# Performance work log

Measured on AMD Instinct MI355X. Metric: run time of the kernel, lower is better.

## Reference

```python
import jax, jax.numpy as jnp
import numpy as np

N_NODES = 100_000
E_OFF = 1_000_000
HID = 32
GF = 8
NF = 8
N_LAYERS = 3


def _mlp(h, W1, b1, W2, b2):
    # Linear -> ReLU -> Linear (matches MLP([in, hidden, out]))
    return jax.nn.relu(h @ W1 + b1) @ W2 + b2


def _seg_mean(v, idx, n):
    s = jax.ops.segment_sum(v, idx, num_segments=n)
    c = jax.ops.segment_sum(jnp.ones((v.shape[0], 1), v.dtype), idx, num_segments=n)
    return s / jnp.maximum(c, 1.0)


def _graphnet(x, row, col, eattr2, g, p):
    # GraphNet with global block: edge MLP -> mean-aggregate to nodes -> node MLP -> global MLP
    eW1, eb1, eW2, eb2, nW1, nb1, nW2, nb2, gW1, gb1, gW2, gb2 = p
    n, e = x.shape[0], row.shape[0]
    gE = jnp.broadcast_to(g, (e, g.shape[1]))
    e_emb = _mlp(jnp.concatenate([gE, x[row], x[col], eattr2], axis=1), eW1, eb1, eW2, eb2)
    agg = _seg_mean(e_emb, row, n)
    gN = jnp.broadcast_to(g, (n, g.shape[1]))
    n_emb = _mlp(jnp.concatenate([gN, x, agg], axis=1), nW1, nb1, nW2, nb2)
    g_new = _mlp(jnp.concatenate([n_emb.mean(0, keepdims=True), e_emb.mean(0, keepdims=True), g], axis=1),
                 gW1, gb1, gW2, gb2)
    return e_emb, n_emb, g_new


def setup_inputs() -> dict:
    key = jax.random.key(0)
    ks = jax.random.split(key, 24)
    a = jax.random.randint(ks[0], (E_OFF,), 0, N_NODES)
    b = jax.random.randint(ks[1], (E_OFF,), 0, N_NODES)
    d = jnp.arange(N_NODES)
    l_ei = jnp.stack([jnp.concatenate([jnp.maximum(a, b), d]),
                      jnp.concatenate([jnp.minimum(a, b), d])])  # lower triangular + diag
    c = jax.random.randint(ks[2], (E_OFF,), 0, N_NODES)
    e = jax.random.randint(ks[3], (E_OFF,), 0, N_NODES)
    u_ei = jnp.stack([jnp.concatenate([jnp.minimum(c, e), d]),
                      jnp.concatenate([jnp.maximum(c, e), d])])  # upper triangular + diag
    E = E_OFF + N_NODES
    x = jax.random.normal(ks[4], (N_NODES, NF), dtype=jnp.float32)
    l_attr = jax.random.normal(ks[5], (E, 1), dtype=jnp.float32)
    u_attr = jax.random.normal(ks[6], (E, 1), dtype=jnp.float32)

    def w(k, shape):
        return (jax.random.normal(k, shape, dtype=jnp.float32) / np.sqrt(shape[-2])).astype(jnp.float32)

    e_in = GF + 2 * NF + 1 + 1  # 26 (edge attr padded to 2: skip col, zeros where absent)
    n_in = GF + 1 + NF          # 17
    g_in = NF + 1 + GF          # 17
    return {
        'x': x, 'l_edge_index': l_ei, 'u_edge_index': u_ei,
        'l_edge_attr': l_attr, 'u_edge_attr': u_attr,
        'eW1': w(ks[7], (2, N_LAYERS, e_in, HID)), 'eb1': 0.01 * jax.random.normal(ks[8], (2, N_LAYERS, HID)),
        'eW2': w(ks[9], (2, N_LAYERS, HID, 1)), 'eb2': 0.01 * jax.random.normal(ks[10], (2, N_LAYERS, 1)),
        'nW1': w(ks[11], (2, N_LAYERS, n_in, HID)), 'nb1': 0.01 * jax.random.normal(ks[12], (2, N_LAYERS, HID)),
        'nW2': w(ks[13], (2, N_LAYERS, HID, NF)), 'nb2': 0.01 * jax.random.normal(ks[14], (2, N_LAYERS, NF)),
        'gW1': w(ks[15], (2, N_LAYERS, g_in, HID)), 'gb1': 0.01 * jax.random.normal(ks[16], (2, N_LAYERS, HID)),
        'gW2': w(ks[17], (2, N_LAYERS, HID, GF)), 'gb2': 0.01 * jax.random.normal(ks[18], (2, N_LAYERS, GF)),
    }


def reference(x, l_edge_index, u_edge_index, l_edge_attr, u_edge_attr,
              eW1, eb1, eW2, eb2, nW1, nb1, nW2, nb2, gW1, gb1, gW2, gb2):
    params = (eW1, eb1, eW2, eb2, nW1, nb1, nW2, nb2, gW1, gb1, gW2, gb2)
    lr, lc = l_edge_index[0], l_edge_index[1]
    ur, uc = u_edge_index[0], u_edge_index[1]
    g = jnp.zeros((1, GF), x.dtype)
    l_e, u_e = l_edge_attr, u_edge_attr
    l_a = l_edge_attr  # skip-connection edge features (original matrix values)
    zl, zu = jnp.zeros_like(l_edge_attr), jnp.zeros_like(u_edge_attr)
    for i in range(N_LAYERS):
        p1 = tuple(w[0, i] for w in params)
        p2 = tuple(w[1, i] for w in params)
        l_in = jnp.concatenate([l_e, l_a if i != 0 else zl], axis=1)  # zeros col == no skip (block 0)
        l_e, l_n, g = _graphnet(x, lr, lc, l_in, g, p1)
        u_in = jnp.concatenate([u_e, zu], axis=1)  # l2 never has skip; padded zeros col
        u_e, u_n, g = _graphnet(l_n, ur, uc, u_in, g, p2)
        # NOTE: node embeddings are NOT carried across MP blocks in the original
    l_vals = jnp.where(lr == lc, jnp.exp(l_e[:, 0]), l_e[:, 0])
    u_vals = jnp.where(ur == uc, jnp.exp(u_e[:, 0]), u_e[:, 0])
    return jnp.concatenate([l_vals, u_vals])
```

## Files before the change

kernel.cpp:

```cpp
#include <hip/hip_runtime.h>


typedef unsigned int u32;
typedef unsigned long long u64;

#define NB_SHIFT 8
#define NB_SIZE 256
#define RSTRIDE 1104

__device__ __forceinline__ float wave_sum(float v) {
#pragma unroll
    for (int off = 32; off > 0; off >>= 1) v += __shfl_down(v, off, 64);
    return v;
}


__global__ __launch_bounds__(512) void hist_kernel(
    const int* __restrict__ lr, const int* __restrict__ ur,
    u32* __restrict__ hist, int E, int B) {
    __shared__ u32 h[512];
    const int t = threadIdx.x;
    if (t < B) h[t] = 0;
    __syncthreads();
    const int s = blockIdx.y;
    const int* rows = s ? ur : lr;
    for (int i = blockIdx.x * 512 + t; i < E; i += gridDim.x * 512)
        atomicAdd(&h[rows[i] >> NB_SHIFT], 1u);
    __syncthreads();
    if (t < B && h[t]) atomicAdd(&hist[s * B + t], h[t]);
}

__global__ __launch_bounds__(512) void scan_kernel(
    const u32* __restrict__ hist, u32* __restrict__ offs,
    u32* __restrict__ cur, int B) {
    __shared__ u32 sh[512];
    const int t = threadIdx.x;
    for (int s = 0; s < 2; ++s) {
        const u32 v = (t < B) ? hist[s * B + t] : 0u;
        sh[t] = v;
        __syncthreads();
#pragma unroll
        for (int off = 1; off < 512; off <<= 1) {
            const u32 add = (t >= off) ? sh[t - off] : 0u;
            __syncthreads();
            sh[t] += add;
            __syncthreads();
        }
        const u32 exc = sh[t] - v;
        if (t < B) {
            offs[s * (B + 1) + t] = exc;
            cur[s * B + t] = exc;
        }
        if (t == 511) offs[s * (B + 1) + B] = sh[511];
        __syncthreads();
    }
}

#define SCHUNK 4096
__global__ __launch_bounds__(512) void scatter_kernel(
    const int* __restrict__ lr, const int* __restrict__ lc,
    const int* __restrict__ ur, const int* __restrict__ uc,
    const float* __restrict__ la, const float* __restrict__ ua,
    u32* __restrict__ cur, uint4* __restrict__ tmp, int E, int B) {
    __shared__ u32 lcnt[512], lbase[512];
    const int t = threadIdx.x;
    const int s = blockIdx.y;
    const int* rows = s ? ur : lr;
    const int* cols = s ? uc : lc;
    const float* attr = s ? ua : la;
    uint4* my = tmp + (size_t)s * E;
    if (t < B) lcnt[t] = 0;
    __syncthreads();
    const int base_e = blockIdx.x * SCHUNK;
#pragma unroll
    for (int k = 0; k < SCHUNK / 512; ++k) {
        const int e = base_e + k * 512 + t;
        if (e < E) atomicAdd(&lcnt[rows[e] >> NB_SHIFT], 1u);
    }
    __syncthreads();
    if (t < B) {
        const u32 c = lcnt[t];
        lbase[t] = c ? atomicAdd(&cur[s * B + t], c) : 0u;
        lcnt[t] = 0;
    }
    __syncthreads();
#pragma unroll
    for (int k = 0; k < SCHUNK / 512; ++k) {
        const int e = base_e + k * 512 + t;
        if (e < E) {
            const int r = rows[e];
            const int b = r >> NB_SHIFT;
            const u32 pos = lbase[b] + atomicAdd(&lcnt[b], 1u);
            my[pos] = make_uint4((u32)r, (u32)cols[e], (u32)e,
                                 __float_as_uint(attr[e]));
        }
    }
}


__global__ __launch_bounds__(512) void sort_kernel(
    const uint4* __restrict__ tmp, u64* __restrict__ ekeys,
    float* __restrict__ eattrs, const u32* __restrict__ offs,
    u32* __restrict__ row_offs, int E, int N, int B) {
    __shared__ u32 cnt[NB_SIZE];
    __shared__ u32 scn[NB_SIZE];
    const int t = threadIdx.x;
    const int s = blockIdx.y;
    const int b = blockIdx.x;
    const uint4* in = tmp + (size_t)s * E;
    u64* okey = ekeys + (size_t)s * E;
    float* oattr = eattrs + (size_t)s * E;
    u32* rofs = row_offs + (size_t)s * (N + 1);
    const u32 beg = offs[s * (B + 1) + b], end = offs[s * (B + 1) + b + 1];
    if (t < NB_SIZE) cnt[t] = 0;
    __syncthreads();
    for (u32 i = beg + t; i < end; i += 512)
        atomicAdd(&cnt[in[i].x & (NB_SIZE - 1)], 1u);
    __syncthreads();
    if (t < NB_SIZE) scn[t] = cnt[t];
    __syncthreads();
#pragma unroll
    for (int off = 1; off < NB_SIZE; off <<= 1) {
        u32 add = 0;
        if (t < NB_SIZE && t >= off) add = scn[t - off];
        __syncthreads();
        if (t < NB_SIZE) scn[t] += add;
        __syncthreads();
    }
    const int n0 = b << NB_SHIFT;
    if (t < NB_SIZE) {
        const u32 excl = scn[t] - cnt[t];
        if (n0 + t < N) rofs[n0 + t] = beg + excl;
        cnt[t] = excl;
    }
    if (b == 0 && t == 0) rofs[N] = (u32)E;
    __syncthreads();
    for (u32 i = beg + t; i < end; i += 512) {
        const uint4 r = in[i];
        const u32 pos = beg + atomicAdd(&cnt[r.x & (NB_SIZE - 1)], 1u);
        okey[pos] = ((u64)r.z << 34) | ((u64)(r.x & 0x1FFFFu) << 17) |
                    (u64)(r.y & 0x1FFFFu);
        oattr[pos] = __uint_as_float(r.w);
    }
}


__global__ __launch_bounds__(256) void atabx_kernel(
    const float4* __restrict__ xf, const float* __restrict__ eW1,
    float4* __restrict__ AtabL, int N) {
    const int n = blockIdx.x * 256 + threadIdx.x;
    if (n >= N) return;
    const float4 x0 = xf[2 * (size_t)n], x1 = xf[2 * (size_t)n + 1];
    const float xs[8] = {x0.x, x0.y, x0.z, x0.w, x1.x, x1.y, x1.z, x1.w};
    for (int m = 0; m < 3; ++m) {
        const float* __restrict__ WA = eW1 + (size_t)m * 832 + 8 * 32;
        float a[32];
#pragma unroll
        for (int j = 0; j < 32; ++j) a[j] = 0.0f;
#pragma unroll
        for (int k = 0; k < 8; ++k) {
            const float v = xs[k];
#pragma unroll
            for (int j = 0; j < 32; ++j) a[j] = fmaf(v, WA[k * 32 + j], a[j]);
        }
        float4* An = AtabL + (size_t)m * 8 * N + 8 * (size_t)n;
#pragma unroll
        for (int q = 0; q < 8; ++q)
            An[q] = make_float4(a[4 * q], a[4 * q + 1], a[4 * q + 2],
                                a[4 * q + 3]);
    }
}


template <bool SKIP, bool FIRST, bool GAGG, bool VALS, bool STORE, bool GCOMP>
__global__ __launch_bounds__(256) void edge_kernel(
    const u64* __restrict__ ekey,
    const float* __restrict__ eattr,
    const float4* __restrict__ Atab,
    const float4* __restrict__ xf,
    const float* __restrict__ eprev,
    const float* __restrict__ W1,
    const float* __restrict__ b1,
    const float* __restrict__ W2,
    const float* __restrict__ b2,
    const float* __restrict__ gprev,
    float* __restrict__ gout,
    const float* __restrict__ pebins,
    const float* __restrict__ pnbins,
    const float* __restrict__ gW1, const float* __restrict__ gb1,
    const float* __restrict__ gW2, const float* __restrict__ gb2,
    float* __restrict__ ebins,
    float* __restrict__ e_out,
    float* __restrict__ vals_out,
    int E, int N, float inv_E, int cpx) {
    __shared__ float gsh[8];
    __shared__ float biasE[32];
    __shared__ float wpart[4];
    const int t = threadIdx.x;
    const int lid = (blockIdx.x & 7) * cpx + (blockIdx.x >> 3);
    const int i0 = lid * 256;
    if (i0 >= E) return;

    if constexpr (GCOMP) {
        if (t < 64) {
            float nb[8];
#pragma unroll
            for (int q = 0; q < 8; ++q) nb[q] = pnbins[t * 16 + q];
            const float eb = pebins[t];
            float gin[17];
#pragma unroll
            for (int q = 0; q < 8; ++q) {
                const float s = wave_sum(nb[q]);
                gin[q] = __shfl(s, 0, 64) / (float)N;
            }
            const float es = wave_sum(eb);
            gin[8] = __shfl(es, 0, 64) * inv_E;
#pragma unroll
            for (int k = 0; k < 8; ++k) gin[9 + k] = gprev[k];
            float hv = 0.0f;
            if (t < 32) {
                hv = gb1[t];
#pragma unroll
                for (int k = 0; k < 17; ++k)
                    hv = fmaf(gin[k], gW1[k * 32 + t], hv);
                hv = fmaxf(hv, 0.0f);
            }
#pragma unroll
            for (int q = 0; q < 8; ++q) {
                const float c = (t < 32) ? hv * gW2[t * 8 + q] : 0.0f;
                const float s = wave_sum(c);
                if (t == 0) {
                    const float gv = gb2[q] + s;
                    gsh[q] = gv;
                    if (blockIdx.x == 0) gout[q] = gv;
                }
            }
        }
    } else {
        if (t < 8) gsh[t] = gprev[t];
    }
    __syncthreads();
    if (t < 32) {
        float v = b1[t];
#pragma unroll
        for (int k = 0; k < 8; ++k) v = fmaf(gsh[k], W1[k * 32 + t], v);
        biasE[t] = v;
    }
    __syncthreads();

    const int i = i0 + t;
    const bool valid = i < E;
    const int idx = valid ? i : i0;

    const u64 key = ekey[idx];
    const u32 c = (u32)key & 0x1FFFFu;
    const u32 r = (u32)(key >> 17) & 0x1FFFFu;
    float attr = 0.0f;
    if constexpr (FIRST || SKIP) attr = eattr[idx];
    float epv;
    if constexpr (FIRST) epv = attr;
    else epv = eprev[idx];
    const float4* __restrict__ Ar = Atab + 8 * (size_t)r;
    float h[32];
#pragma unroll
    for (int q = 0; q < 8; ++q) {
        const float4 av = Ar[q];
        const float4 bi = reinterpret_cast<const float4*>(biasE)[q];
        h[4 * q + 0] = bi.x + av.x; h[4 * q + 1] = bi.y + av.y;
        h[4 * q + 2] = bi.z + av.z; h[4 * q + 3] = bi.w + av.w;
    }
    const float4 xc0 = xf[2 * (size_t)c], xc1 = xf[2 * (size_t)c + 1];
    const float cx[8] = {xc0.x, xc0.y, xc0.z, xc0.w,
                         xc1.x, xc1.y, xc1.z, xc1.w};
    const float* __restrict__ Wc = W1 + 16 * 32;
#pragma unroll
    for (int k = 0; k < 8; ++k) {
        const float v = cx[k];
#pragma unroll
        for (int j = 0; j < 32; ++j) h[j] = fmaf(v, Wc[k * 32 + j], h[j]);
    }
    const float* __restrict__ W24 = W1 + 24 * 32;
#pragma unroll
    for (int j = 0; j < 32; ++j) h[j] = fmaf(epv, W24[j], h[j]);
    if constexpr (SKIP) {
        const float* __restrict__ W25 = W1 + 25 * 32;
#pragma unroll
        for (int j = 0; j < 32; ++j) h[j] = fmaf(attr, W25[j], h[j]);
    }
    float out = b2[0];
#pragma unroll
    for (int j = 0; j < 32; ++j) out = fmaf(fmaxf(h[j], 0.0f), W2[j], out);

    if (valid) {
        if constexpr (STORE) e_out[i] = out;
        if constexpr (VALS) {
            const u32 eid = (u32)(key >> 34);
            vals_out[eid] = (r == c) ? expf(out) : out;
        }
    }
    if constexpr (GAGG) {
        const float s = wave_sum(valid ? out : 0.0f);
        if ((t & 63) == 0) wpart[t >> 6] = s;
        __syncthreads();
        if (t == 0)
            atomicAdd(&ebins[lid & 63],
                      wpart[0] + wpart[1] + wpart[2] + wpart[3]);
    }
}


template <bool EVEN>
__global__ __launch_bounds__(256) void nodemlp_kernel(
    const float* __restrict__ ep,
    const u32* __restrict__ row_offs,
    const float4* __restrict__ xf,
    const float* __restrict__ g,
    const float* __restrict__ nW1, const float* __restrict__ nb1,
    const float* __restrict__ nW2, const float* __restrict__ nb2,
    float* __restrict__ n_out,
    float* __restrict__ nbins,
    const float* __restrict__ W1u,
    float4* __restrict__ AtabU,
    int N, int cpn) {
    __shared__ float biasN[32];
    __shared__ float npart[4][8];
    const int t = threadIdx.x;
    if (t < 32) {
        float v = nb1[t];
#pragma unroll
        for (int k = 0; k < 8; ++k) v = fmaf(g[k], nW1[k * 32 + t], v);
        biasN[t] = v;
    }
    __syncthreads();
    const int lid = (blockIdx.x & 7) * cpn + (blockIdx.x >> 3);
    const int n = lid * 256 + t;
    const bool active = n < N;
    const int idx = active ? n : (N - 1);
    const u32 beg = row_offs[idx], end = row_offs[idx + 1];
    float ssum = 0.0f;
    for (u32 i = beg; i < end; ++i) ssum += ep[i];
    const float agg = ssum / fmaxf((float)(end - beg), 1.0f);
    const float4 x0 = xf[2 * (size_t)idx], x1 = xf[2 * (size_t)idx + 1];
    float in[9] = {x0.x, x0.y, x0.z, x0.w, x1.x, x1.y, x1.z, x1.w, agg};
    float h[32];
#pragma unroll
    for (int j = 0; j < 8; ++j) {
        const float4 bb = reinterpret_cast<const float4*>(biasN)[j];
        h[4 * j + 0] = bb.x; h[4 * j + 1] = bb.y;
        h[4 * j + 2] = bb.z; h[4 * j + 3] = bb.w;
    }
    const float* __restrict__ Wk = nW1 + 8 * 32;
#pragma unroll
    for (int k = 0; k < 9; ++k) {
        const float v = in[k];
#pragma unroll
        for (int j = 0; j < 32; ++j) h[j] = fmaf(v, Wk[k * 32 + j], h[j]);
    }
    float o[8];
#pragma unroll
    for (int q = 0; q < 8; ++q) o[q] = nb2[q];
#pragma unroll
    for (int j = 0; j < 32; ++j) {
        const float hv = fmaxf(h[j], 0.0f);
#pragma unroll
        for (int q = 0; q < 8; ++q) o[q] = fmaf(hv, nW2[j * 8 + q], o[q]);
    }
    if constexpr (EVEN) {
        if (active) {
            reinterpret_cast<float4*>(n_out)[2 * n] =
                make_float4(o[0], o[1], o[2], o[3]);
            reinterpret_cast<float4*>(n_out)[2 * n + 1] =
                make_float4(o[4], o[5], o[6], o[7]);
            const float* __restrict__ WA = W1u + 8 * 32;
            float a[32];
#pragma unroll
            for (int j = 0; j < 32; ++j) a[j] = 0.0f;
#pragma unroll
            for (int k = 0; k < 8; ++k) {
                const float v = o[k];
#pragma unroll
                for (int j = 0; j < 32; ++j)
                    a[j] = fmaf(v, WA[k * 32 + j], a[j]);
            }
            float4* An = AtabU + 8 * (size_t)n;
#pragma unroll
            for (int q = 0; q < 8; ++q)
                An[q] = make_float4(a[4 * q], a[4 * q + 1], a[4 * q + 2],
                                    a[4 * q + 3]);
        }
    }
#pragma unroll
    for (int q = 0; q < 8; ++q) {
        const float s2 = wave_sum(active ? o[q] : 0.0f);
        if ((t & 63) == 0) npart[t >> 6][q] = s2;
    }
    __syncthreads();
    if (t < 8) {
        float a = 0.0f;
#pragma unroll
        for (int w = 0; w < 4; ++w) a += npart[w][t];
        atomicAdd(&nbins[(blockIdx.x & 63) * 16 + t], a);
    }
}

extern "C" void kernel_launch(void* const* d_in, const int* in_sizes, int n_in,
                              void* d_out, int out_size, void* d_ws,
                              size_t ws_size, hipStream_t stream) {
    const float* x = (const float*)d_in[0];
    const int* l_ei = (const int*)d_in[1];
    const int* u_ei = (const int*)d_in[2];
    const float* l_attr = (const float*)d_in[3];
    const float* u_attr = (const float*)d_in[4];
    const float* eW1 = (const float*)d_in[5];
    const float* eb1 = (const float*)d_in[6];
    const float* eW2 = (const float*)d_in[7];
    const float* eb2 = (const float*)d_in[8];
    const float* nW1 = (const float*)d_in[9];
    const float* nb1 = (const float*)d_in[10];
    const float* nW2 = (const float*)d_in[11];
    const float* nb2 = (const float*)d_in[12];
    const float* gW1 = (const float*)d_in[13];
    const float* gb1 = (const float*)d_in[14];
    const float* gW2 = (const float*)d_in[15];
    const float* gb2 = (const float*)d_in[16];

    const int E = in_sizes[3];
    const int N = in_sizes[0] / 8;
    const int B = (N + NB_SIZE - 1) >> NB_SHIFT;
    const int Ep = (E + 3) & ~3;

    u64* ekeys = (u64*)d_ws;
    float* eattrs = (float*)(ekeys + (size_t)2 * E);
    uint4* tmp = (uint4*)(eattrs + (size_t)2 * E);
    float* AtabU = (float*)tmp;
    float* l_e = AtabU + (size_t)32 * N;
    float* u_e = l_e + Ep;
    float* l_n = u_e + Ep;
    float* AtabL = (float*)(tmp + (size_t)2 * E);
    float* gslot = AtabL + (size_t)96 * N;
    u32* hist = (u32*)(gslot + 56);
    float* dyn_all = (float*)(hist + 2 * B);
    u32* offs = (u32*)(dyn_all + 5 * RSTRIDE);
    u32* cur = offs + 2 * (B + 1);
    u32* row_offs = cur + 2 * B;

    const int* lr = l_ei;
    const int* lc = l_ei + E;
    const int* ur = u_ei;
    const int* uc = u_ei + E;
    const int sg = (E + SCHUNK - 1) / SCHUNK;
    const int ng = (N + 255) / 256;
    const int ngp = (ng + 7) & ~7;
    const int cpn = ngp >> 3;
    const int eg = (E + 255) / 256;
    const int nwg8 = (eg + 7) & ~7;
    const int cpx = nwg8 >> 3;
    const float invE = 1.0f / (float)E;
    float* outL = (float*)d_out;
    float* outU = outL + E;

    hipMemsetAsync(gslot, 0, (size_t)(56 + 2 * B + 5 * RSTRIDE) * sizeof(float),
                   stream);
    hist_kernel<<<dim3(64, 2), 512, 0, stream>>>(lr, ur, hist, E, B);
    scan_kernel<<<1, 512, 0, stream>>>(hist, offs, cur, B);
    scatter_kernel<<<dim3(sg, 2), 512, 0, stream>>>(lr, lc, ur, uc, l_attr,
                                                    u_attr, cur, tmp, E, B);
    sort_kernel<<<dim3(B, 2), 512, 0, stream>>>(tmp, ekeys, eattrs, offs,
                                                row_offs, E, N, B);
    atabx_kernel<<<ng, 256, 0, stream>>>((const float4*)x, eW1,
                                         (float4*)AtabL, N);

    const size_t wsl[6] = {0, 3, 1, 4, 2, 5};

    for (int j = 0; j < 6; ++j) {
        const bool lower = !(j & 1);
        const size_t sl = wsl[j];
        float* ebins = dyn_all + (size_t)(j <= 4 ? j : 4) * RSTRIDE;
        float* nbins = ebins + 64;
        const float* pe = (j >= 1) ? dyn_all + (size_t)(j - 1) * RSTRIDE : nullptr;
        const float* pn = (j >= 1) ? pe + 64 : nullptr;
        const size_t psl = (j >= 1) ? wsl[j - 1] : 0;
        const float4* exf = (const float4*)(lower ? x : l_n);
        const u64* ekey_t = ekeys + (size_t)(lower ? 0 : 1) * E;
        const float* eattr_t = eattrs + (size_t)(lower ? 0 : 1) * E;
        const u32* roffs = row_offs + (size_t)(lower ? 0 : 1) * (N + 1);
        const float* eprev = lower ? l_e : u_e;
        float* e_out = lower ? l_e : u_e;
        const float* gprev = gslot + (size_t)(j >= 1 ? j - 1 : 0) * 8;
        float* gout = gslot + (size_t)j * 8;
        const float* Atab_j =
            lower ? AtabL + (size_t)(j >> 1) * 32 * N : AtabU;

#define EDGE_ARGS                                                             \
    ekey_t, eattr_t, (const float4*)Atab_j, exf, eprev, eW1 + sl * 832,       \
        eb1 + sl * 32, eW2 + sl * 32, eb2 + sl, gprev, gout, pe, pn,          \
        gW1 + psl * 544, gb1 + psl * 32, gW2 + psl * 256, gb2 + psl * 8,      \
        ebins, e_out, (j == 4) ? outL : outU, E, N, invE, cpx

        switch (j) {
            case 0: edge_kernel<false, true, true, false, true, false>
                        <<<nwg8, 256, 0, stream>>>(EDGE_ARGS); break;
            case 1: edge_kernel<false, true, true, false, true, true>
                        <<<nwg8, 256, 0, stream>>>(EDGE_ARGS); break;
            case 2: edge_kernel<true, false, true, false, true, true>
                        <<<nwg8, 256, 0, stream>>>(EDGE_ARGS); break;
            case 3: edge_kernel<false, false, true, false, true, true>
                        <<<nwg8, 256, 0, stream>>>(EDGE_ARGS); break;
            case 4: edge_kernel<true, false, true, true, true, true>
                        <<<nwg8, 256, 0, stream>>>(EDGE_ARGS); break;
            case 5: edge_kernel<false, false, false, true, false, true>
                        <<<nwg8, 256, 0, stream>>>(EDGE_ARGS); break;
        }
#undef EDGE_ARGS

        if (j == 5) break;

#define NODE_ARGS                                                             \
    e_out, roffs, exf, gslot + (size_t)j * 8, nW1 + sl * 544, nb1 + sl * 32,  \
        nW2 + sl * 256, nb2 + sl * 8, l_n, nbins,                             \
        eW1 + wsl[j + 1] * 832, (float4*)AtabU, N, cpn

        switch (j) {
            case 0: nodemlp_kernel<true>
                        <<<ngp, 256, 0, stream>>>(NODE_ARGS); break;
            case 1: nodemlp_kernel<false>
                        <<<ngp, 256, 0, stream>>>(NODE_ARGS); break;
            case 2: nodemlp_kernel<true>
                        <<<ngp, 256, 0, stream>>>(NODE_ARGS); break;
            case 3: nodemlp_kernel<false>
                        <<<ngp, 256, 0, stream>>>(NODE_ARGS); break;
            case 4: nodemlp_kernel<true>
                        <<<ngp, 256, 0, stream>>>(NODE_ARGS); break;
        }
#undef NODE_ARGS
    }
}
```

Measured before the change: 489.9 us.

## Fuse per-layer edge/node kernels into one persistent kernel with grid barriers

Replaces the atabx kernel and the eleven per-stage edge and node-MLP launches with one persistent kernel. Blocks loop over work with grid-stride loops and meet at software grid barriers built from global atomics. The aim is to remove launch gaps and tail effects between the many small dependent stages. In exchange, each barrier costs a spin wait, template specialisation is lost so the stage flags become runtime branches, and the grid size must be capped to the number of co-resident blocks or the barrier can deadlock.

```diff
diff --git a/kernel.cpp b/kernel.cpp
--- a/kernel.cpp
+++ b/kernel.cpp
@@ -12,6 +12,23 @@
 #pragma unroll
     for (int off = 32; off > 0; off >>= 1) v += __shfl_down(v, off, 64);
     return v;
+}
+
+__device__ __forceinline__ void gbar(u32* __restrict__ bar) {
+    __threadfence();
+    __syncthreads();
+    if (threadIdx.x == 0) {
+        const u32 g0 = atomicAdd(&bar[1], 0u);
+        if (atomicAdd(&bar[0], 1u) == gridDim.x - 1u) {
+            atomicExch(&bar[0], 0u);
+            __threadfence();
+            atomicAdd(&bar[1], 1u);
+        } else {
+            while (atomicAdd(&bar[1], 0u) == g0) __builtin_amdgcn_s_sleep(8);
+        }
+    }
+    __syncthreads();
+    __threadfence();
 }
 
 
@@ -145,261 +162,303 @@
 }
 
 
-__global__ __launch_bounds__(256) void atabx_kernel(
-    const float4* __restrict__ xf, const float* __restrict__ eW1,
-    float4* __restrict__ AtabL, int N) {
-    const int n = blockIdx.x * 256 + threadIdx.x;
-    if (n >= N) return;
-    const float4 x0 = xf[2 * (size_t)n], x1 = xf[2 * (size_t)n + 1];
-    const float xs[8] = {x0.x, x0.y, x0.z, x0.w, x1.x, x1.y, x1.z, x1.w};
-    for (int m = 0; m < 3; ++m) {
-        const float* __restrict__ WA = eW1 + (size_t)m * 832 + 8 * 32;
-        float a[32];
-#pragma unroll
-        for (int j = 0; j < 32; ++j) a[j] = 0.0f;
-#pragma unroll
-        for (int k = 0; k < 8; ++k) {
-            const float v = xs[k];
-#pragma unroll
-            for (int j = 0; j < 32; ++j) a[j] = fmaf(v, WA[k * 32 + j], a[j]);
-        }
-        float4* An = AtabL + (size_t)m * 8 * N + 8 * (size_t)n;
-#pragma unroll
-        for (int q = 0; q < 8; ++q)
-            An[q] = make_float4(a[4 * q], a[4 * q + 1], a[4 * q + 2],
-                                a[4 * q + 3]);
-    }
-}
-
-
-template <bool SKIP, bool FIRST, bool GAGG, bool VALS, bool STORE, bool GCOMP>
-__global__ __launch_bounds__(256) void edge_kernel(
-    const u64* __restrict__ ekey,
-    const float* __restrict__ eattr,
-    const float4* __restrict__ Atab,
-    const float4* __restrict__ xf,
-    const float* __restrict__ eprev,
-    const float* __restrict__ W1,
-    const float* __restrict__ b1,
-    const float* __restrict__ W2,
-    const float* __restrict__ b2,
-    const float* __restrict__ gprev,
-    float* __restrict__ gout,
-    const float* __restrict__ pebins,
-    const float* __restrict__ pnbins,
+__global__ __launch_bounds__(256, 4) void fused_kernel(
+    const u64* __restrict__ ekeys, const float* __restrict__ eattrs,
+    float* __restrict__ AtabL, float* __restrict__ AtabU,
+    const float4* __restrict__ xF, float* __restrict__ l_e,
+    float* __restrict__ u_e, float* __restrict__ l_n,
+    const float* __restrict__ eW1, const float* __restrict__ eb1,
+    const float* __restrict__ eW2, const float* __restrict__ eb2,
+    const float* __restrict__ nW1, const float* __restrict__ nb1,
+    const float* __restrict__ nW2, const float* __restrict__ nb2,
     const float* __restrict__ gW1, const float* __restrict__ gb1,
     const float* __restrict__ gW2, const float* __restrict__ gb2,
-    float* __restrict__ ebins,
-    float* __restrict__ e_out,
-    float* __restrict__ vals_out,
-    int E, int N, float inv_E, int cpx) {
+    float* __restrict__ gslot, float* __restrict__ dyn_all,
+    u32* __restrict__ bar, const u32* __restrict__ row_offs,
+    float* __restrict__ outL, float* __restrict__ outU, int E, int N,
+    float inv_E, int EG, int cpx, int NG, int cpn, int ng) {
+    const int t = threadIdx.x;
+    const int nblk = (int)gridDim.x;
     __shared__ float gsh[8];
     __shared__ float biasE[32];
     __shared__ float wpart[4];
-    const int t = threadIdx.x;
-    const int lid = (blockIdx.x & 7) * cpx + (blockIdx.x >> 3);
-    const int i0 = lid * 256;
-    if (i0 >= E) return;
-
-    if constexpr (GCOMP) {
-        if (t < 64) {
-            float nb[8];
-#pragma unroll
-            for (int q = 0; q < 8; ++q) nb[q] = pnbins[t * 16 + q];
-            const float eb = pebins[t];
-            float gin[17];
-#pragma unroll
-            for (int q = 0; q < 8; ++q) {
-                const float s = wave_sum(nb[q]);
-                gin[q] = __shfl(s, 0, 64) / (float)N;
-            }
-            const float es = wave_sum(eb);
-            gin[8] = __shfl(es, 0, 64) * inv_E;
-#pragma unroll
-            for (int k = 0; k < 8; ++k) gin[9 + k] = gprev[k];
-            float hv = 0.0f;
-            if (t < 32) {
-                hv = gb1[t];
-#pragma unroll
-                for (int k = 0; k < 17; ++k)
-                    hv = fmaf(gin[k], gW1[k * 32 + t], hv);
-                hv = fmaxf(hv, 0.0f);
-            }
-#pragma unroll
-            for (int q = 0; q < 8; ++q) {
-                const float c = (t < 32) ? hv * gW2[t * 8 + q] : 0.0f;
-                const float s = wave_sum(c);
-                if (t == 0) {
-                    const float gv = gb2[q] + s;
-                    gsh[q] = gv;
-                    if (blockIdx.x == 0) gout[q] = gv;
-                }
-            }
-        }
-    } else {
-        if (t < 8) gsh[t] = gprev[t];
-    }
-    __syncthreads();
-    if (t < 32) {
-        float v = b1[t];
-#pragma unroll
-        for (int k = 0; k < 8; ++k) v = fmaf(gsh[k], W1[k * 32 + t], v);
-        biasE[t] = v;
-    }
-    __syncthreads();
-
-    const int i = i0 + t;
-    const bool valid = i < E;
-    const int idx = valid ? i : i0;
-
-    const u64 key = ekey[idx];
-    const u32 c = (u32)key & 0x1FFFFu;
-    const u32 r = (u32)(key >> 17) & 0x1FFFFu;
-    float attr = 0.0f;
-    if constexpr (FIRST || SKIP) attr = eattr[idx];
-    float epv;
-    if constexpr (FIRST) epv = attr;
-    else epv = eprev[idx];
-    const float4* __restrict__ Ar = Atab + 8 * (size_t)r;
-    float h[32];
-#pragma unroll
-    for (int q = 0; q < 8; ++q) {
-        const float4 av = Ar[q];
-        const float4 bi = reinterpret_cast<const float4*>(biasE)[q];
-        h[4 * q + 0] = bi.x + av.x; h[4 * q + 1] = bi.y + av.y;
-        h[4 * q + 2] = bi.z + av.z; h[4 * q + 3] = bi.w + av.w;
-    }
-    const float4 xc0 = xf[2 * (size_t)c], xc1 = xf[2 * (size_t)c + 1];
-    const float cx[8] = {xc0.x, xc0.y, xc0.z, xc0.w,
-                         xc1.x, xc1.y, xc1.z, xc1.w};
-    const float* __restrict__ Wc = W1 + 16 * 32;
-#pragma unroll
-    for (int k = 0; k < 8; ++k) {
-        const float v = cx[k];
-#pragma unroll
-        for (int j = 0; j < 32; ++j) h[j] = fmaf(v, Wc[k * 32 + j], h[j]);
-    }
-    const float* __restrict__ W24 = W1 + 24 * 32;
-#pragma unroll
-    for (int j = 0; j < 32; ++j) h[j] = fmaf(epv, W24[j], h[j]);
-    if constexpr (SKIP) {
-        const float* __restrict__ W25 = W1 + 25 * 32;
-#pragma unroll
-        for (int j = 0; j < 32; ++j) h[j] = fmaf(attr, W25[j], h[j]);
-    }
-    float out = b2[0];
-#pragma unroll
-    for (int j = 0; j < 32; ++j) out = fmaf(fmaxf(h[j], 0.0f), W2[j], out);
-
-    if (valid) {
-        if constexpr (STORE) e_out[i] = out;
-        if constexpr (VALS) {
-            const u32 eid = (u32)(key >> 34);
-            vals_out[eid] = (r == c) ? expf(out) : out;
-        }
-    }
-    if constexpr (GAGG) {
-        const float s = wave_sum(valid ? out : 0.0f);
-        if ((t & 63) == 0) wpart[t >> 6] = s;
-        __syncthreads();
-        if (t == 0)
-            atomicAdd(&ebins[lid & 63],
-                      wpart[0] + wpart[1] + wpart[2] + wpart[3]);
-    }
-}
-
-
-template <bool EVEN>
-__global__ __launch_bounds__(256) void nodemlp_kernel(
-    const float* __restrict__ ep,
-    const u32* __restrict__ row_offs,
-    const float4* __restrict__ xf,
-    const float* __restrict__ g,
-    const float* __restrict__ nW1, const float* __restrict__ nb1,
-    const float* __restrict__ nW2, const float* __restrict__ nb2,
-    float* __restrict__ n_out,
-    float* __restrict__ nbins,
-    const float* __restrict__ W1u,
-    float4* __restrict__ AtabU,
-    int N, int cpn) {
     __shared__ float biasN[32];
     __shared__ float npart[4][8];
-    const int t = threadIdx.x;
-    if (t < 32) {
-        float v = nb1[t];
-#pragma unroll
-        for (int k = 0; k < 8; ++k) v = fmaf(g[k], nW1[k * 32 + t], v);
-        biasN[t] = v;
-    }
-    __syncthreads();
-    const int lid = (blockIdx.x & 7) * cpn + (blockIdx.x >> 3);
-    const int n = lid * 256 + t;
-    const bool active = n < N;
-    const int idx = active ? n : (N - 1);
-    const u32 beg = row_offs[idx], end = row_offs[idx + 1];
-    float ssum = 0.0f;
-    for (u32 i = beg; i < end; ++i) ssum += ep[i];
-    const float agg = ssum / fmaxf((float)(end - beg), 1.0f);
-    const float4 x0 = xf[2 * (size_t)idx], x1 = xf[2 * (size_t)idx + 1];
-    float in[9] = {x0.x, x0.y, x0.z, x0.w, x1.x, x1.y, x1.z, x1.w, agg};
-    float h[32];
-#pragma unroll
-    for (int j = 0; j < 8; ++j) {
-        const float4 bb = reinterpret_cast<const float4*>(biasN)[j];
-        h[4 * j + 0] = bb.x; h[4 * j + 1] = bb.y;
-        h[4 * j + 2] = bb.z; h[4 * j + 3] = bb.w;
-    }
-    const float* __restrict__ Wk = nW1 + 8 * 32;
-#pragma unroll
-    for (int k = 0; k < 9; ++k) {
-        const float v = in[k];
-#pragma unroll
-        for (int j = 0; j < 32; ++j) h[j] = fmaf(v, Wk[k * 32 + j], h[j]);
-    }
-    float o[8];
-#pragma unroll
-    for (int q = 0; q < 8; ++q) o[q] = nb2[q];
-#pragma unroll
-    for (int j = 0; j < 32; ++j) {
-        const float hv = fmaxf(h[j], 0.0f);
-#pragma unroll
-        for (int q = 0; q < 8; ++q) o[q] = fmaf(hv, nW2[j * 8 + q], o[q]);
-    }
-    if constexpr (EVEN) {
-        if (active) {
-            reinterpret_cast<float4*>(n_out)[2 * n] =
-                make_float4(o[0], o[1], o[2], o[3]);
-            reinterpret_cast<float4*>(n_out)[2 * n + 1] =
-                make_float4(o[4], o[5], o[6], o[7]);
-            const float* __restrict__ WA = W1u + 8 * 32;
+
+    for (int vb = blockIdx.x; vb < ng; vb += nblk) {
+        const int n = vb * 256 + t;
+        if (n >= N) continue;
+        const float4 x0 = xF[2 * (size_t)n], x1 = xF[2 * (size_t)n + 1];
+        const float xs[8] = {x0.x, x0.y, x0.z, x0.w,
+                             x1.x, x1.y, x1.z, x1.w};
+        for (int m = 0; m < 3; ++m) {
+            const float* __restrict__ WA = eW1 + (size_t)m * 832 + 8 * 32;
             float a[32];
 #pragma unroll
             for (int j = 0; j < 32; ++j) a[j] = 0.0f;
 #pragma unroll
             for (int k = 0; k < 8; ++k) {
-                const float v = o[k];
+                const float v = xs[k];
 #pragma unroll
                 for (int j = 0; j < 32; ++j)
                     a[j] = fmaf(v, WA[k * 32 + j], a[j]);
             }
-            float4* An = AtabU + 8 * (size_t)n;
+            float4* An =
+                (float4*)AtabL + (size_t)m * 8 * N + 8 * (size_t)n;
 #pragma unroll
             for (int q = 0; q < 8; ++q)
                 An[q] = make_float4(a[4 * q], a[4 * q + 1], a[4 * q + 2],
                                     a[4 * q + 3]);
         }
     }
-#pragma unroll
-    for (int q = 0; q < 8; ++q) {
-        const float s2 = wave_sum(active ? o[q] : 0.0f);
-        if ((t & 63) == 0) npart[t >> 6][q] = s2;
-    }
-    __syncthreads();
-    if (t < 8) {
-        float a = 0.0f;
-#pragma unroll
-        for (int w = 0; w < 4; ++w) a += npart[w][t];
-        atomicAdd(&nbins[(blockIdx.x & 63) * 16 + t], a);
+    gbar(bar);
+
+    const int wsl[6] = {0, 3, 1, 4, 2, 5};
+    for (int j = 0; j < 6; ++j) {
+        const bool lower = !(j & 1);
+        const bool SKIP = (j == 2) || (j == 4);
+        const bool FIRST = (j <= 1);
+        const bool GAGG = (j < 5);
+        const bool VALS = (j >= 4);
+        const bool STORE = (j < 5);
+        const bool GCOMP = (j >= 1);
+        const int sl = wsl[j];
+        const int psl = (j >= 1) ? wsl[j - 1] : 0;
+        const float* __restrict__ W1 = eW1 + (size_t)sl * 832;
+        const float* __restrict__ b1v = eb1 + (size_t)sl * 32;
+        const float* __restrict__ W2 = eW2 + (size_t)sl * 32;
+        const float* __restrict__ b2v = eb2 + sl;
+        float* ebins = dyn_all + (size_t)j * RSTRIDE;
+        const float* pe =
+            (j >= 1) ? dyn_all + (size_t)(j - 1) * RSTRIDE : nullptr;
+        const float* pn = (j >= 1) ? pe + 64 : nullptr;
+        const float* gprev = gslot + (size_t)(j >= 1 ? j - 1 : 0) * 8;
+        float* gout = gslot + (size_t)j * 8;
+        const u64* __restrict__ ekey = ekeys + (size_t)(lower ? 0 : 1) * E;
+        const float* __restrict__ eattr =
+            eattrs + (size_t)(lower ? 0 : 1) * E;
+        const float4* __restrict__ Atab =
+            (const float4*)(lower ? AtabL + (size_t)(j >> 1) * 32 * N
+                                  : AtabU);
+        const float4* __restrict__ xf =
+            lower ? xF : (const float4*)l_n;
+        const float* __restrict__ eprev = lower ? l_e : u_e;
+        float* __restrict__ e_out = lower ? l_e : u_e;
+        float* __restrict__ vals_out = (j == 4) ? outL : outU;
+        const float* gW1j = gW1 + (size_t)psl * 544;
+        const float* gb1j = gb1 + (size_t)psl * 32;
+        const float* gW2j = gW2 + (size_t)psl * 256;
+        const float* gb2j = gb2 + (size_t)psl * 8;
+
+        if (GCOMP) {
+            if (t < 64) {
+                float nb[8];
+#pragma unroll
+                for (int q = 0; q < 8; ++q) nb[q] = pn[t * 16 + q];
+                const float eb = pe[t];
+                float gin[17];
+#pragma unroll
+                for (int q = 0; q < 8; ++q) {
+                    const float s = wave_sum(nb[q]);
+                    gin[q] = __shfl(s, 0, 64) / (float)N;
+                }
+                const float es = wave_sum(eb);
+                gin[8] = __shfl(es, 0, 64) * inv_E;
+#pragma unroll
+                for (int k = 0; k < 8; ++k) gin[9 + k] = gprev[k];
+                float hv = 0.0f;
+                if (t < 32) {
+                    hv = gb1j[t];
+#pragma unroll
+                    for (int k = 0; k < 17; ++k)
+                        hv = fmaf(gin[k], gW1j[k * 32 + t], hv);
+                    hv = fmaxf(hv, 0.0f);
+                }
+#pragma unroll
+                for (int q = 0; q < 8; ++q) {
+                    const float c = (t < 32) ? hv * gW2j[t * 8 + q] : 0.0f;
+                    const float s = wave_sum(c);
+                    if (t == 0) {
+                        const float gv = gb2j[q] + s;
+                        gsh[q] = gv;
+                        if (blockIdx.x == 0) gout[q] = gv;
+                    }
+                }
+            }
+        } else {
+            if (t < 8) gsh[t] = gprev[t];
+        }
+        __syncthreads();
+        if (t < 32) {
+            float v = b1v[t];
+#pragma unroll
+            for (int k = 0; k < 8; ++k) v = fmaf(gsh[k], W1[k * 32 + t], v);
+            biasE[t] = v;
+        }
+        __syncthreads();
+
+        for (int vb = blockIdx.x; vb < EG; vb += nblk) {
+            const int lid = (vb & 7) * cpx + (vb >> 3);
+            const int i0 = lid * 256;
+            if (i0 >= E) continue;
+            const int i = i0 + t;
+            const bool valid = i < E;
+            const int idx = valid ? i : i0;
+            const u64 key = ekey[idx];
+            const u32 c = (u32)key & 0x1FFFFu;
+            const u32 r = (u32)(key >> 17) & 0x1FFFFu;
+            float attr = 0.0f;
+            if (FIRST || SKIP) attr = eattr[idx];
+            float epv;
+            if (FIRST) epv = attr;
+            else epv = eprev[idx];
+            const float4* __restrict__ Ar = Atab + 8 * (size_t)r;
+            float h[32];
+#pragma unroll
+            for (int q = 0; q < 8; ++q) {
+                const float4 av = Ar[q];
+                const float4 bi = reinterpret_cast<const float4*>(biasE)[q];
+                h[4 * q + 0] = bi.x + av.x; h[4 * q + 1] = bi.y + av.y;
+                h[4 * q + 2] = bi.z + av.z; h[4 * q + 3] = bi.w + av.w;
+            }
+            const float4 xc0 = xf[2 * (size_t)c];
+            const float4 xc1 = xf[2 * (size_t)c + 1];
+            const float cx[8] = {xc0.x, xc0.y, xc0.z, xc0.w,
+                                 xc1.x, xc1.y, xc1.z, xc1.w};
+            const float* __restrict__ Wc = W1 + 16 * 32;
+#pragma unroll
+            for (int k = 0; k < 8; ++k) {
+                const float v = cx[k];
+#pragma unroll
+                for (int jj = 0; jj < 32; ++jj)
+                    h[jj] = fmaf(v, Wc[k * 32 + jj], h[jj]);
+            }
+            const float* __restrict__ W24 = W1 + 24 * 32;
+#pragma unroll
+            for (int jj = 0; jj < 32; ++jj)
+                h[jj] = fmaf(epv, W24[jj], h[jj]);
+            if (SKIP) {
+                const float* __restrict__ W25 = W1 + 25 * 32;
+#pragma unroll
+                for (int jj = 0; jj < 32; ++jj)
+                    h[jj] = fmaf(attr, W25[jj], h[jj]);
+            }
+            float out = b2v[0];
+#pragma unroll
+            for (int jj = 0; jj < 32; ++jj)
+                out = fmaf(fmaxf(h[jj], 0.0f), W2[jj], out);
+            if (valid) {
+                if (STORE) e_out[i] = out;
+                if (VALS) {
+                    const u32 eid = (u32)(key >> 34);
+                    vals_out[eid] = (r == c) ? expf(out) : out;
+                }
+            }
+            if (GAGG) {
+                const float s = wave_sum(valid ? out : 0.0f);
+                if ((t & 63) == 0) wpart[t >> 6] = s;
+                __syncthreads();
+                if (t == 0)
+                    atomicAdd(&ebins[lid & 63],
+                              wpart[0] + wpart[1] + wpart[2] + wpart[3]);
+                __syncthreads();
+            }
+        }
+        gbar(bar);
+        if (j == 5) break;
+
+        const bool EVEN = lower;
+        const float* __restrict__ nW1j = nW1 + (size_t)sl * 544;
+        const float* __restrict__ nb1j = nb1 + (size_t)sl * 32;
+        const float* __restrict__ nW2j = nW2 + (size_t)sl * 256;
+        const float* __restrict__ nb2j = nb2 + (size_t)sl * 8;
+        const float* gj = gslot + (size_t)j * 8;
+        float* nbins = ebins + 64;
+        const u32* __restrict__ roffs =
+            row_offs + (size_t)(lower ? 0 : 1) * (N + 1);
+        const float* __restrict__ W1u = eW1 + (size_t)wsl[j + 1] * 832;
+        if (t < 32) {
+            float v = nb1j[t];
+#pragma unroll
+            for (int k = 0; k < 8; ++k) v = fmaf(gj[k], nW1j[k * 32 + t], v);
+            biasN[t] = v;
+        }
+        __syncthreads();
+        for (int vb = blockIdx.x; vb < NG; vb += nblk) {
+            const int lid = (vb & 7) * cpn + (vb >> 3);
+            const int n = lid * 256 + t;
+            const bool active = n < N;
+            const int idx = active ? n : (N - 1);
+            const u32 beg = roffs[idx], end = roffs[idx + 1];
+            float ssum = 0.0f;
+            for (u32 i2 = beg; i2 < end; ++i2) ssum += e_out[i2];
+            const float agg = ssum / fmaxf((float)(end - beg), 1.0f);
+            const float4 x0 = xf[2 * (size_t)idx];
+            const float4 x1 = xf[2 * (size_t)idx + 1];
+            float in[9] = {x0.x, x0.y, x0.z, x0.w,
+                           x1.x, x1.y, x1.z, x1.w, agg};
+            float h[32];
+#pragma unroll
+            for (int jj = 0; jj < 8; ++jj) {
+                const float4 bb = reinterpret_cast<const float4*>(biasN)[jj];
+                h[4 * jj + 0] = bb.x; h[4 * jj + 1] = bb.y;
+                h[4 * jj + 2] = bb.z; h[4 * jj + 3] = bb.w;
+            }
+            const float* __restrict__ Wk = nW1j + 8 * 32;
+#pragma unroll
+            for (int k = 0; k < 9; ++k) {
+                const float v = in[k];
+#pragma unroll
+                for (int jj = 0; jj < 32; ++jj)
+                    h[jj] = fmaf(v, Wk[k * 32 + jj], h[jj]);
+            }
+            float o[8];
+#pragma unroll
+            for (int q = 0; q < 8; ++q) o[q] = nb2j[q];
+#pragma unroll
+            for (int jj = 0; jj < 32; ++jj) {
+                const float hv = fmaxf(h[jj], 0.0f);
+#pragma unroll
+                for (int q = 0; q < 8; ++q)
+                    o[q] = fmaf(hv, nW2j[jj * 8 + q], o[q]);
+            }
+            if (EVEN && active) {
+                reinterpret_cast<float4*>(l_n)[2 * n] =
+                    make_float4(o[0], o[1], o[2], o[3]);
+                reinterpret_cast<float4*>(l_n)[2 * n + 1] =
+                    make_float4(o[4], o[5], o[6], o[7]);
+                const float* __restrict__ WA = W1u + 8 * 32;
+                float a[32];
+#pragma unroll
+                for (int jj = 0; jj < 32; ++jj) a[jj] = 0.0f;
+#pragma unroll
+                for (int k = 0; k < 8; ++k) {
+                    const float v = o[k];
+#pragma unroll
+                    for (int jj = 0; jj < 32; ++jj)
+                        a[jj] = fmaf(v, WA[k * 32 + jj], a[jj]);
+                }
+                float4* An = (float4*)AtabU + 8 * (size_t)n;
+#pragma unroll
+                for (int q = 0; q < 8; ++q)
+                    An[q] = make_float4(a[4 * q], a[4 * q + 1],
+                                        a[4 * q + 2], a[4 * q + 3]);
+            }
+#pragma unroll
+            for (int q = 0; q < 8; ++q) {
+                const float s2 = wave_sum(active ? o[q] : 0.0f);
+                if ((t & 63) == 0) npart[t >> 6][q] = s2;
+            }
+            __syncthreads();
+            if (t < 8) {
+                float a = 0.0f;
+#pragma unroll
+                for (int w = 0; w < 4; ++w) a += npart[w][t];
+                atomicAdd(&nbins[(vb & 63) * 16 + t], a);
+            }
+            __syncthreads();
+        }
+        gbar(bar);
     }
 }
 
@@ -440,7 +499,8 @@
     float* gslot = AtabL + (size_t)96 * N;
     u32* hist = (u32*)(gslot + 56);
     float* dyn_all = (float*)(hist + 2 * B);
-    u32* offs = (u32*)(dyn_all + 5 * RSTRIDE);
+    u32* bar = (u32*)(dyn_all + 6 * RSTRIDE);
+    u32* offs = bar + 8;
     u32* cur = offs + 2 * (B + 1);
     u32* row_offs = cur + 2 * B;
 
@@ -459,7 +519,8 @@
     float* outL = (float*)d_out;
     float* outU = outL + E;
 
-    hipMemsetAsync(gslot, 0, (size_t)(56 + 2 * B + 5 * RSTRIDE) * sizeof(float),
+    hipMemsetAsync(gslot, 0,
+                   (size_t)(56 + 2 * B + 6 * RSTRIDE + 8) * sizeof(float),
                    stream);
     hist_kernel<<<dim3(64, 2), 512, 0, stream>>>(lr, ur, hist, E, B);
     scan_kernel<<<1, 512, 0, stream>>>(hist, offs, cur, B);
@@ -467,71 +528,18 @@
                                                     u_attr, cur, tmp, E, B);
     sort_kernel<<<dim3(B, 2), 512, 0, stream>>>(tmp, ekeys, eattrs, offs,
                                                 row_offs, E, N, B);
-    atabx_kernel<<<ng, 256, 0, stream>>>((const float4*)x, eW1,
-                                         (float4*)AtabL, N);
-
-    const size_t wsl[6] = {0, 3, 1, 4, 2, 5};
-
-    for (int j = 0; j < 6; ++j) {
-        const bool lower = !(j & 1);
-        const size_t sl = wsl[j];
-        float* ebins = dyn_all + (size_t)(j <= 4 ? j : 4) * RSTRIDE;
-        float* nbins = ebins + 64;
-        const float* pe = (j >= 1) ? dyn_all + (size_t)(j - 1) * RSTRIDE : nullptr;
-        const float* pn = (j >= 1) ? pe + 64 : nullptr;
-        const size_t psl = (j >= 1) ? wsl[j - 1] : 0;
-        const float4* exf = (const float4*)(lower ? x : l_n);
-        const u64* ekey_t = ekeys + (size_t)(lower ? 0 : 1) * E;
-        const float* eattr_t = eattrs + (size_t)(lower ? 0 : 1) * E;
-        const u32* roffs = row_offs + (size_t)(lower ? 0 : 1) * (N + 1);
-        const float* eprev = lower ? l_e : u_e;
-        float* e_out = lower ? l_e : u_e;
-        const float* gprev = gslot + (size_t)(j >= 1 ? j - 1 : 0) * 8;
-        float* gout = gslot + (size_t)j * 8;
-        const float* Atab_j =
-            lower ? AtabL + (size_t)(j >> 1) * 32 * N : AtabU;
-
-#define EDGE_ARGS                                                             \
-    ekey_t, eattr_t, (const float4*)Atab_j, exf, eprev, eW1 + sl * 832,       \
-        eb1 + sl * 32, eW2 + sl * 32, eb2 + sl, gprev, gout, pe, pn,          \
-        gW1 + psl * 544, gb1 + psl * 32, gW2 + psl * 256, gb2 + psl * 8,      \
-        ebins, e_out, (j == 4) ? outL : outU, E, N, invE, cpx
-
-        switch (j) {
-            case 0: edge_kernel<false, true, true, false, true, false>
-                        <<<nwg8, 256, 0, stream>>>(EDGE_ARGS); break;
-            case 1: edge_kernel<false, true, true, false, true, true>
-                        <<<nwg8, 256, 0, stream>>>(EDGE_ARGS); break;
-            case 2: edge_kernel<true, false, true, false, true, true>
-                        <<<nwg8, 256, 0, stream>>>(EDGE_ARGS); break;
-            case 3: edge_kernel<false, false, true, false, true, true>
-                        <<<nwg8, 256, 0, stream>>>(EDGE_ARGS); break;
-            case 4: edge_kernel<true, false, true, true, true, true>
-                        <<<nwg8, 256, 0, stream>>>(EDGE_ARGS); break;
-            case 5: edge_kernel<false, false, false, true, false, true>
-                        <<<nwg8, 256, 0, stream>>>(EDGE_ARGS); break;
-        }
-#undef EDGE_ARGS
-
-        if (j == 5) break;
-
-#define NODE_ARGS                                                             \
-    e_out, roffs, exf, gslot + (size_t)j * 8, nW1 + sl * 544, nb1 + sl * 32,  \
-        nW2 + sl * 256, nb2 + sl * 8, l_n, nbins,                             \
-        eW1 + wsl[j + 1] * 832, (float4*)AtabU, N, cpn
-
-        switch (j) {
-            case 0: nodemlp_kernel<true>
-                        <<<ngp, 256, 0, stream>>>(NODE_ARGS); break;
-            case 1: nodemlp_kernel<false>
-                        <<<ngp, 256, 0, stream>>>(NODE_ARGS); break;
-            case 2: nodemlp_kernel<true>
-                        <<<ngp, 256, 0, stream>>>(NODE_ARGS); break;
-            case 3: nodemlp_kernel<false>
-                        <<<ngp, 256, 0, stream>>>(NODE_ARGS); break;
-            case 4: nodemlp_kernel<true>
-                        <<<ngp, 256, 0, stream>>>(NODE_ARGS); break;
-        }
-#undef NODE_ARGS
-    }
-}
+
+    int maxPerCU = 0;
+    int nblk = 1024;
+    if (hipOccupancyMaxActiveBlocksPerMultiprocessor(
+            &maxPerCU, (const void*)fused_kernel, 256, 0) == hipSuccess &&
+        maxPerCU >= 1) {
+        const int cap = maxPerCU * 256;
+        if (cap < nblk) nblk = cap;
+    }
+    fused_kernel<<<nblk, 256, 0, stream>>>(
+        ekeys, eattrs, AtabL, AtabU, (const float4*)x, l_e, u_e, l_n, eW1,
+        eb1, eW2, eb2, nW1, nb1, nW2, nb2, gW1, gb1, gW2, gb2, gslot,
+        dyn_all, bar, row_offs, outL, outU, E, N, invE, nwg8, cpx, ngp, cpn,
+        ng);
+}
```

After: 1.741 ms. +255.3%, slower.
